# Kernel optimization log

Measured on AMD Instinct MI355X. Metric: run time of the kernel, lower is better.

The kernel has to match this reference:

```python
import jax, jax.numpy as jnp
import numpy as np

N_NODES = 50000
N_EDGES = 600000
D = 128


def setup_inputs() -> dict:
    key = jax.random.key(0)
    ks = jax.random.split(key, 8)
    s = 0.05
    return {
        "x": jax.random.normal(ks[0], (N_NODES, D), jnp.float32),
        "edge_index": jax.random.randint(ks[1], (2, N_EDGES), 0, N_NODES, jnp.int64),
        "edge_attr": jax.random.normal(ks[2], (N_EDGES, D), jnp.float32),
        "We1": jax.random.normal(ks[3], (3 * D, D), jnp.float32) * s,
        "be1": jnp.zeros((D,), jnp.float32),
        "We2": jax.random.normal(ks[4], (D, D), jnp.float32) * s,
        "be2": jnp.zeros((D,), jnp.float32),
        "Wn1": jax.random.normal(ks[5], (2 * D, D), jnp.float32) * s,
        "bn1": jnp.zeros((D,), jnp.float32),
        "Wn2": jax.random.normal(ks[6], (D, D), jnp.float32) * s,
        "bn2": jnp.zeros((D,), jnp.float32),
    }


def reference(x, edge_index, edge_attr, We1, be1, We2, be2, Wn1, bn1, Wn2, bn2):
    src = edge_index[0]
    dest = edge_index[1]
    n = x.shape[0]
    # edge model: MLP on [x_src | x_dest | edge_attr]  -> [E, D]
    e_in = jnp.concatenate([x[src], x[dest], edge_attr], axis=-1)
    e = jax.nn.relu(e_in @ We1 + be1) @ We2 + be2
    # node model: scatter-mean of updated edge_attr into dest nodes
    agg = jax.ops.segment_sum(e, dest, num_segments=n)
    cnt = jax.ops.segment_sum(jnp.ones((e.shape[0],), e.dtype), dest, num_segments=n)
    agg = agg / jnp.maximum(cnt, 1.0)[:, None]
    n_in = jnp.concatenate([x, agg], axis=-1)
    x_out = jax.nn.relu(n_in @ Wn1 + bn1) @ Wn2 + bn2
    return x_out, e
```

## Files before the change

kernel.cpp:

```cpp
#include <hip/hip_runtime.h>
#include <hip/hip_bf16.h>

#define DD 128

typedef short bf16x8 __attribute__((ext_vector_type(8)));
typedef float f32x4 __attribute__((ext_vector_type(4)));

__device__ __forceinline__ unsigned short f2b(float f) {
  unsigned int u = __float_as_uint(f);
  u = u + 0x7FFFu + ((u >> 16) & 1u);
  return (unsigned short)(u >> 16);
}
__device__ __forceinline__ float b2f(unsigned short u) {
  return __uint_as_float((unsigned int)u << 16);
}

__global__ void count_kernel(const int* __restrict__ ei, int* __restrict__ cnt, int E) {
  int i = blockIdx.x * blockDim.x + threadIdx.x;
  if (i < E) atomicAdd(&cnt[ei[E + i]], 1);
}

__global__ __launch_bounds__(256) void scan_a(const int* __restrict__ cnt,
                                              int* __restrict__ off,
                                              int* __restrict__ bsum, int N) {
  __shared__ int wsum[4];
  const int t = threadIdx.x;
  const int i0 = blockIdx.x * 1024 + t * 4;
  int4 v = {0, 0, 0, 0};
  if (i0 + 3 < N) v = *reinterpret_cast<const int4*>(cnt + i0);
  else {
    if (i0 < N)     v.x = cnt[i0];
    if (i0 + 1 < N) v.y = cnt[i0 + 1];
    if (i0 + 2 < N) v.z = cnt[i0 + 2];
    if (i0 + 3 < N) v.w = cnt[i0 + 3];
  }
  const int s1 = v.x, s2 = s1 + v.y, s3 = s2 + v.z, tot = s3 + v.w;
  const int lane = t & 63, wv = t >> 6;
  int sc = tot;
#pragma unroll
  for (int d = 1; d < 64; d <<= 1) {
    int u = __shfl_up(sc, d);
    if (lane >= d) sc += u;
  }
  if (lane == 63) wsum[wv] = sc;
  __syncthreads();
  int wpre = 0;
  for (int w = 0; w < wv; ++w) wpre += wsum[w];
  const int excl = wpre + sc - tot;
  if (i0 < N)     off[i0]     = excl;
  if (i0 + 1 < N) off[i0 + 1] = excl + s1;
  if (i0 + 2 < N) off[i0 + 2] = excl + s2;
  if (i0 + 3 < N) off[i0 + 3] = excl + s3;
  if (t == 255) bsum[blockIdx.x] = wpre + sc;
}

__global__ void scan_b(int* __restrict__ bsum, int B) {
  const int t = threadIdx.x;
  const int v0 = (t < B) ? bsum[t] : 0;
  int v = v0;
#pragma unroll
  for (int d = 1; d < 64; d <<= 1) {
    int u = __shfl_up(v, d);
    if (t >= d) v += u;
  }
  if (t < B) bsum[t] = v - v0;
}

__global__ __launch_bounds__(256) void scan_c(int* __restrict__ off, int* __restrict__ cur,
                                              const int* __restrict__ bsum, int N, int E) {
  const int t = threadIdx.x;
  const int add = bsum[blockIdx.x];
  const int i0 = blockIdx.x * 1024 + t * 4;
#pragma unroll
  for (int k = 0; k < 4; ++k) {
    const int i = i0 + k;
    if (i < N) {
      const int o = off[i] + add;
      off[i] = o;
      cur[i] = o;
    }
  }
  if (blockIdx.x == 0 && t == 0) off[N] = E;
}

__global__ void fill_kernel(const int* __restrict__ ei, int* __restrict__ cur,
                            int* __restrict__ perm, int E) {
  int i = blockIdx.x * blockDim.x + threadIdx.x;
  if (i < E) {
    const int d = ei[E + i];
    const int pos = atomicAdd(&cur[d], 1);
    perm[pos] = i;
  }
}

__global__ __launch_bounds__(256, 2) void pq_kernel(
    const float* __restrict__ x,
    const float* __restrict__ We1,
    unsigned short* __restrict__ pq,
    int N)
{
  __shared__ __align__(16) unsigned short x_lds[64][128];

  const int tid  = threadIdx.x;
  const int wv   = tid >> 6;
  const int lane = tid & 63;
  const int lg   = lane >> 4;
  const int lm   = lane & 15;

  bf16x8 wf[4][4];
#pragma unroll
  for (int nf = 0; nf < 4; ++nf) {
    const int n    = wv * 64 + nf * 16 + lm;
    const int col  = n & 127;
    const int kro  = (n >> 7) * 128;
#pragma unroll
    for (int kb = 0; kb < 4; ++kb) {
      bf16x8 f;
#pragma unroll
      for (int j = 0; j < 8; ++j)
        f[j] = (short)f2b(We1[(kro + kb * 32 + lg * 8 + j) * DD + col]);
      wf[kb][nf] = f;
    }
  }

  const int nbase = blockIdx.x * 64;

#pragma unroll
  for (int it = 0; it < 4; ++it) {
    const int q = tid + it * 256;
    const int r = q >> 4;
    const int c = q & 15;
    int gr = nbase + r; if (gr >= N) gr = N - 1;
    const float* p = x + (size_t)gr * DD + c * 8;
    const float4 va = *reinterpret_cast<const float4*>(p);
    const float4 vb = *reinterpret_cast<const float4*>(p + 4);
    bf16x8 o;
    o[0] = (short)f2b(va.x); o[1] = (short)f2b(va.y);
    o[2] = (short)f2b(va.z); o[3] = (short)f2b(va.w);
    o[4] = (short)f2b(vb.x); o[5] = (short)f2b(vb.y);
    o[6] = (short)f2b(vb.z); o[7] = (short)f2b(vb.w);
    *reinterpret_cast<bf16x8*>(&x_lds[r][(c ^ (r & 7)) * 8]) = o;
  }
  __syncthreads();

  f32x4 acc[4][4];
#pragma unroll
  for (int mf = 0; mf < 4; ++mf)
#pragma unroll
    for (int nf = 0; nf < 4; ++nf)
      acc[mf][nf] = (f32x4){0.f, 0.f, 0.f, 0.f};

#pragma unroll
  for (int kb = 0; kb < 4; ++kb) {
    bf16x8 a[4];
#pragma unroll
    for (int mf = 0; mf < 4; ++mf) {
      const int r = mf * 16 + lm;
      a[mf] = *reinterpret_cast<const bf16x8*>(&x_lds[r][((kb * 4 + lg) ^ (r & 7)) * 8]);
    }
#pragma unroll
    for (int mf = 0; mf < 4; ++mf)
#pragma unroll
      for (int nf = 0; nf < 4; ++nf)
        acc[mf][nf] = __builtin_amdgcn_mfma_f32_16x16x32_bf16(a[mf], wf[kb][nf], acc[mf][nf], 0, 0, 0);
  }

#pragma unroll
  for (int mf = 0; mf < 4; ++mf)
#pragma unroll
    for (int rg = 0; rg < 4; ++rg) {
      const int gm = nbase + mf * 16 + lg * 4 + rg;
      if (gm < N) {
#pragma unroll
        for (int nf = 0; nf < 4; ++nf)
          pq[(size_t)gm * 256 + wv * 64 + nf * 16 + lm] = f2b(acc[mf][nf][rg]);
      }
    }
}

__global__ __launch_bounds__(256, 3) void edge_mlp_kernel(
    const unsigned short* __restrict__ pq,
    const int* __restrict__ ei,
    const float* __restrict__ ea,
    const float* __restrict__ We1,
    const float* __restrict__ be1,
    const float* __restrict__ We2,
    const float* __restrict__ be2,
    float* __restrict__ e_out,
    int E)
{
  __shared__ __align__(16) unsigned short ea_lds[64][128];
  __shared__ __align__(16) unsigned short h_lds[64][136];
  __shared__ int srcs[64], dsts[64];

  const int tid  = threadIdx.x;
  const int wv   = tid >> 6;
  const int lane = tid & 63;
  const int lg   = lane >> 4;
  const int lm   = lane & 15;

  bf16x8 w1f[4][2];
  bf16x8 w2f[4][2];
  float b1[2], b2[2];
#pragma unroll
  for (int nf = 0; nf < 2; ++nf) {
    const int n = wv * 32 + nf * 16 + lm;
    b1[nf] = be1[n];
    b2[nf] = be2[n];
#pragma unroll
    for (int kb = 0; kb < 4; ++kb) {
      bf16x8 f;
#pragma unroll
      for (int j = 0; j < 8; ++j)
        f[j] = (short)f2b(We1[(256 + kb * 32 + lg * 8 + j) * DD + n]);
      w1f[kb][nf] = f;
    }
#pragma unroll
    for (int kb = 0; kb < 4; ++kb) {
      bf16x8 f;
#pragma unroll
      for (int j = 0; j < 8; ++j)
        f[j] = (short)f2b(We2[(kb * 32 + lg * 8 + j) * DD + n]);
      w2f[kb][nf] = f;
    }
  }

  const int ntiles = E >> 6;
  for (int tile = blockIdx.x; tile < ntiles; tile += gridDim.x) {
    const int ebase = tile << 6;
    __syncthreads();

    if (tid < 64)       srcs[tid]      = ei[ebase + tid];
    else if (tid < 128) dsts[tid - 64] = ei[E + ebase + tid - 64];
    __syncthreads();

    float4 va[4], vb[4];
#pragma unroll
    for (int it = 0; it < 4; ++it) {
      const int q = tid + it * 256;
      const float* p = ea + (size_t)(ebase + (q >> 4)) * DD + (q & 15) * 8;
      va[it] = *reinterpret_cast<const float4*>(p);
      vb[it] = *reinterpret_cast<const float4*>(p + 4);
    }

    f32x4 acc[4][2];
#pragma unroll
    for (int mf = 0; mf < 4; ++mf)
#pragma unroll
      for (int rg = 0; rg < 4; ++rg) {
        const int m = mf * 16 + lg * 4 + rg;
        const size_t rs = (size_t)srcs[m] * 256;
        const size_t rd = (size_t)dsts[m] * 256;
#pragma unroll
        for (int nf = 0; nf < 2; ++nf) {
          const int n = wv * 32 + nf * 16 + lm;
          acc[mf][nf][rg] = b2f(pq[rs + n]) + b2f(pq[rd + 128 + n]);
        }
      }

#pragma unroll
    for (int it = 0; it < 4; ++it) {
      const int q = tid + it * 256;
      const int r = q >> 4;
      const int c = q & 15;
      bf16x8 o;
      o[0] = (short)f2b(va[it].x); o[1] = (short)f2b(va[it].y);
      o[2] = (short)f2b(va[it].z); o[3] = (short)f2b(va[it].w);
      o[4] = (short)f2b(vb[it].x); o[5] = (short)f2b(vb[it].y);
      o[6] = (short)f2b(vb[it].z); o[7] = (short)f2b(vb[it].w);
      *reinterpret_cast<bf16x8*>(&ea_lds[r][(c ^ (r & 7)) * 8]) = o;
    }
    __syncthreads();

#pragma unroll
    for (int kb = 0; kb < 4; ++kb) {
      bf16x8 a[4];
#pragma unroll
      for (int mf = 0; mf < 4; ++mf) {
        const int r = mf * 16 + lm;
        a[mf] = *reinterpret_cast<const bf16x8*>(&ea_lds[r][((kb * 4 + lg) ^ (r & 7)) * 8]);
      }
#pragma unroll
      for (int mf = 0; mf < 4; ++mf)
#pragma unroll
        for (int nf = 0; nf < 2; ++nf)
          acc[mf][nf] = __builtin_amdgcn_mfma_f32_16x16x32_bf16(a[mf], w1f[kb][nf], acc[mf][nf], 0, 0, 0);
    }

#pragma unroll
    for (int mf = 0; mf < 4; ++mf)
#pragma unroll
      for (int nf = 0; nf < 2; ++nf)
#pragma unroll
        for (int rg = 0; rg < 4; ++rg) {
          const int m = mf * 16 + lg * 4 + rg;
          const int n = wv * 32 + nf * 16 + lm;
          float v = acc[mf][nf][rg] + b1[nf];
          h_lds[m][n] = f2b(v > 0.f ? v : 0.f);
        }
    __syncthreads();

    f32x4 acc2[4][2];
#pragma unroll
    for (int mf = 0; mf < 4; ++mf)
#pragma unroll
      for (int nf = 0; nf < 2; ++nf)
        acc2[mf][nf] = (f32x4){0.f, 0.f, 0.f, 0.f};

#pragma unroll
    for (int kb = 0; kb < 4; ++kb) {
      bf16x8 a[4];
#pragma unroll
      for (int mf = 0; mf < 4; ++mf)
        a[mf] = *reinterpret_cast<const bf16x8*>(&h_lds[mf * 16 + lm][kb * 32 + lg * 8]);
#pragma unroll
      for (int mf = 0; mf < 4; ++mf)
#pragma unroll
        for (int nf = 0; nf < 2; ++nf)
          acc2[mf][nf] = __builtin_amdgcn_mfma_f32_16x16x32_bf16(a[mf], w2f[kb][nf], acc2[mf][nf], 0, 0, 0);
    }

#pragma unroll
    for (int mf = 0; mf < 4; ++mf)
#pragma unroll
      for (int rg = 0; rg < 4; ++rg) {
        const int gm = ebase + mf * 16 + lg * 4 + rg;
#pragma unroll
        for (int nf = 0; nf < 2; ++nf) {
          const int n = wv * 32 + nf * 16 + lm;
          e_out[(size_t)gm * DD + n] = acc2[mf][nf][rg] + b2[nf];
        }
      }
  }
}

__global__ __launch_bounds__(256) void agg_kernel(const float* __restrict__ e_out,
                                                  const int* __restrict__ off,
                                                  const int* __restrict__ perm,
                                                  float* __restrict__ agg, int N) {
  const int wv   = threadIdx.x >> 6;
  const int lane = threadIdx.x & 63;
  const int nid  = blockIdx.x * 4 + wv;
  if (nid >= N) return;
  const int o0 = off[nid], o1 = off[nid + 1];
  float2 s0 = {0.f, 0.f}, s1 = {0.f, 0.f}, s2 = {0.f, 0.f}, s3 = {0.f, 0.f};
  int j = o0;
  for (; j + 4 <= o1; j += 4) {
    const int r0 = perm[j], r1 = perm[j + 1], r2 = perm[j + 2], r3 = perm[j + 3];
    const float2 v0 = *reinterpret_cast<const float2*>(e_out + (size_t)r0 * DD + (lane << 1));
    const float2 v1 = *reinterpret_cast<const float2*>(e_out + (size_t)r1 * DD + (lane << 1));
    const float2 v2 = *reinterpret_cast<const float2*>(e_out + (size_t)r2 * DD + (lane << 1));
    const float2 v3 = *reinterpret_cast<const float2*>(e_out + (size_t)r3 * DD + (lane << 1));
    s0.x += v0.x; s0.y += v0.y;
    s1.x += v1.x; s1.y += v1.y;
    s2.x += v2.x; s2.y += v2.y;
    s3.x += v3.x; s3.y += v3.y;
  }
  for (; j < o1; ++j) {
    const int r = perm[j];
    const float2 v = *reinterpret_cast<const float2*>(e_out + (size_t)r * DD + (lane << 1));
    s0.x += v.x; s0.y += v.y;
  }
  const int deg = o1 - o0;
  const float inv = deg > 0 ? 1.f / (float)deg : 0.f;
  float2 o;
  o.x = (s0.x + s1.x + s2.x + s3.x) * inv;
  o.y = (s0.y + s1.y + s2.y + s3.y) * inv;
  *reinterpret_cast<float2*>(agg + (size_t)nid * DD + (lane << 1)) = o;
}

__global__ __launch_bounds__(256, 2) void node_mlp_kernel(
    const float* __restrict__ x,
    const float* __restrict__ Wn1,
    const float* __restrict__ bn1,
    const float* __restrict__ Wn2,
    const float* __restrict__ bn2,
    float* __restrict__ xout,
    int N)
{
  __shared__ __align__(16) unsigned short A_lds[64][264];
  __shared__ __align__(16) unsigned short h_lds[64][136];

  const int tid  = threadIdx.x;
  const int wv   = tid >> 6;
  const int lane = tid & 63;
  const int lg   = lane >> 4;
  const int lm   = lane & 15;

  bf16x8 w1f[8][2];
  bf16x8 w2f[4][2];
  float b1[2], b2[2];
#pragma unroll
  for (int nf = 0; nf < 2; ++nf) {
    const int n = wv * 32 + nf * 16 + lm;
    b1[nf] = bn1[n];
    b2[nf] = bn2[n];
#pragma unroll
    for (int kb = 0; kb < 8; ++kb) {
      bf16x8 f;
#pragma unroll
      for (int j = 0; j < 8; ++j)
        f[j] = (short)f2b(Wn1[(kb * 32 + lg * 8 + j) * DD + n]);
      w1f[kb][nf] = f;
    }
#pragma unroll
    for (int kb = 0; kb < 4; ++kb) {
      bf16x8 f;
#pragma unroll
      for (int j = 0; j < 8; ++j)
        f[j] = (short)f2b(Wn2[(kb * 32 + lg * 8 + j) * DD + n]);
      w2f[kb][nf] = f;
    }
  }

  const int ntiles = (N + 63) >> 6;
  for (int tile = blockIdx.x; tile < ntiles; tile += gridDim.x) {
    const int nbase = tile << 6;
    __syncthreads();

#pragma unroll
    for (int it = 0; it < 16; ++it) {
      const int q = tid + it * 256;
      const int r = q >> 6;
      const int c = q & 63;
      int gr = nbase + r;
      if (gr >= N) gr = N - 1;
      float4 v;
      if (c < 32) v = *reinterpret_cast<const float4*>(x + (size_t)gr * DD + (c << 2));
      else        v = *reinterpret_cast<const float4*>(xout + (size_t)gr * DD + ((c - 32) << 2));
      unsigned short* dst = &A_lds[r][c << 2];
      dst[0] = f2b(v.x); dst[1] = f2b(v.y); dst[2] = f2b(v.z); dst[3] = f2b(v.w);
    }
    __syncthreads();

    f32x4 acc[4][2];
#pragma unroll
    for (int mf = 0; mf < 4; ++mf)
#pragma unroll
      for (int nf = 0; nf < 2; ++nf)
        acc[mf][nf] = (f32x4){0.f, 0.f, 0.f, 0.f};

#pragma unroll
    for (int kb = 0; kb < 8; ++kb) {
      bf16x8 a[4];
#pragma unroll
      for (int mf = 0; mf < 4; ++mf)
        a[mf] = *reinterpret_cast<const bf16x8*>(&A_lds[mf * 16 + lm][kb * 32 + lg * 8]);
#pragma unroll
      for (int mf = 0; mf < 4; ++mf)
#pragma unroll
        for (int nf = 0; nf < 2; ++nf)
          acc[mf][nf] = __builtin_amdgcn_mfma_f32_16x16x32_bf16(a[mf], w1f[kb][nf], acc[mf][nf], 0, 0, 0);
    }

#pragma unroll
    for (int mf = 0; mf < 4; ++mf)
#pragma unroll
      for (int nf = 0; nf < 2; ++nf)
#pragma unroll
        for (int rg = 0; rg < 4; ++rg) {
          const int m = mf * 16 + lg * 4 + rg;
          const int n = wv * 32 + nf * 16 + lm;
          float v = acc[mf][nf][rg] + b1[nf];
          h_lds[m][n] = f2b(v > 0.f ? v : 0.f);
        }
    __syncthreads();

    f32x4 acc2[4][2];
#pragma unroll
    for (int mf = 0; mf < 4; ++mf)
#pragma unroll
      for (int nf = 0; nf < 2; ++nf)
        acc2[mf][nf] = (f32x4){0.f, 0.f, 0.f, 0.f};

#pragma unroll
    for (int kb = 0; kb < 4; ++kb) {
      bf16x8 a[4];
#pragma unroll
      for (int mf = 0; mf < 4; ++mf)
        a[mf] = *reinterpret_cast<const bf16x8*>(&h_lds[mf * 16 + lm][kb * 32 + lg * 8]);
#pragma unroll
      for (int mf = 0; mf < 4; ++mf)
#pragma unroll
        for (int nf = 0; nf < 2; ++nf)
          acc2[mf][nf] = __builtin_amdgcn_mfma_f32_16x16x32_bf16(a[mf], w2f[kb][nf], acc2[mf][nf], 0, 0, 0);
    }

#pragma unroll
    for (int mf = 0; mf < 4; ++mf)
#pragma unroll
      for (int rg = 0; rg < 4; ++rg) {
        const int gm = nbase + mf * 16 + lg * 4 + rg;
        if (gm < N) {
#pragma unroll
          for (int nf = 0; nf < 2; ++nf) {
            const int n = wv * 32 + nf * 16 + lm;
            xout[(size_t)gm * DD + n] = acc2[mf][nf][rg] + b2[nf];
          }
        }
      }
  }
}

extern "C" void kernel_launch(void* const* d_in, const int* in_sizes, int n_in,
                              void* d_out, int out_size, void* d_ws, size_t ws_size,
                              hipStream_t stream) {
  const float* x   = (const float*)d_in[0];
  const int*   ei  = (const int*)d_in[1];
  const float* ea  = (const float*)d_in[2];
  const float* We1 = (const float*)d_in[3];
  const float* be1 = (const float*)d_in[4];
  const float* We2 = (const float*)d_in[5];
  const float* be2 = (const float*)d_in[6];
  const float* Wn1 = (const float*)d_in[7];
  const float* bn1 = (const float*)d_in[8];
  const float* Wn2 = (const float*)d_in[9];
  const float* bn2 = (const float*)d_in[10];

  const int N = in_sizes[0] / DD;
  const int E = in_sizes[2] / DD;

  float* out   = (float*)d_out;
  float* xout  = out;
  float* e_out = out + (size_t)N * DD;

  unsigned short* pq = (unsigned short*)xout;

  int* cnt  = (int*)d_ws;
  int* off  = cnt + N;
  int* cur  = off + N + 1;
  int* perm = cur + N;
  int* bsum = perm + E;

  const int SCAN_B = (N + 1023) / 1024;

  hipMemsetAsync(cnt, 0, (size_t)N * sizeof(int), stream);

  pq_kernel<<<(N + 63) / 64, 256, 0, stream>>>(x, We1, pq, N);

  count_kernel<<<(E + 255) / 256, 256, 0, stream>>>(ei, cnt, E);
  scan_a<<<SCAN_B, 256, 0, stream>>>(cnt, off, bsum, N);
  scan_b<<<1, 64, 0, stream>>>(bsum, SCAN_B);
  scan_c<<<SCAN_B, 256, 0, stream>>>(off, cur, bsum, N, E);
  fill_kernel<<<(E + 255) / 256, 256, 0, stream>>>(ei, cur, perm, E);

  edge_mlp_kernel<<<2048, 256, 0, stream>>>(pq, ei, ea, We1, be1, We2, be2, e_out, E);

  agg_kernel<<<(N + 3) / 4, 256, 0, stream>>>(e_out, off, perm, xout, N);

  const int node_tiles = (N + 63) / 64;
  node_mlp_kernel<<<node_tiles, 256, 0, stream>>>(x, Wn1, bn1, Wn2, bn2, xout, N);
}
```

Measured before the change: 401.5 us.

## Transpose edge MLP MFMA operands for vectorized gathers and stores, prefetch indices

Swaps the A and B operands of the edge-MLP MFMAs so each lane holds four consecutive output columns of one edge row. This lets the pq gathers, bias loads and e_out stores use 4-wide vector accesses instead of scalar ones. The hidden-activation LDS buffer now uses an XOR swizzle instead of padding. Edge indices are double-buffered and prefetched for the next tile, which drops one barrier per iteration. Edge-attribute loads move inline to cut register use, and occupancy is raised from 3 to 4 blocks per SM, which risks register spills.

```diff
diff --git a/kernel.cpp b/kernel.cpp
--- a/kernel.cpp
+++ b/kernel.cpp
@@ -4,6 +4,7 @@
 #define DD 128
 
 typedef short bf16x8 __attribute__((ext_vector_type(8)));
+typedef short bf16x4 __attribute__((ext_vector_type(4)));
 typedef float f32x4 __attribute__((ext_vector_type(4)));
 
 __device__ __forceinline__ unsigned short f2b(float f) {
@@ -178,7 +179,7 @@
     }
 }
 
-__global__ __launch_bounds__(256, 3) void edge_mlp_kernel(
+__global__ __launch_bounds__(256, 4) void edge_mlp_kernel(
     const unsigned short* __restrict__ pq,
     const int* __restrict__ ei,
     const float* __restrict__ ea,
@@ -190,8 +191,8 @@
     int E)
 {
   __shared__ __align__(16) unsigned short ea_lds[64][128];
-  __shared__ __align__(16) unsigned short h_lds[64][136];
-  __shared__ int srcs[64], dsts[64];
+  __shared__ __align__(16) unsigned short h_lds[64][128];
+  __shared__ int srcs[2][64], dsts[2][64];
 
   const int tid  = threadIdx.x;
   const int wv   = tid >> 6;
@@ -201,12 +202,12 @@
 
   bf16x8 w1f[4][2];
   bf16x8 w2f[4][2];
-  float b1[2], b2[2];
+  float4 b1v[2], b2v[2];
 #pragma unroll
   for (int nf = 0; nf < 2; ++nf) {
     const int n = wv * 32 + nf * 16 + lm;
-    b1[nf] = be1[n];
-    b2[nf] = be2[n];
+    b1v[nf] = *reinterpret_cast<const float4*>(&be1[wv * 32 + nf * 16 + 4 * lg]);
+    b2v[nf] = *reinterpret_cast<const float4*>(&be2[wv * 32 + nf * 16 + 4 * lg]);
 #pragma unroll
     for (int kb = 0; kb < 4; ++kb) {
       bf16x8 f;
@@ -226,49 +227,61 @@
   }
 
   const int ntiles = E >> 6;
-  for (int tile = blockIdx.x; tile < ntiles; tile += gridDim.x) {
+
+  {
+    const int t0 = blockIdx.x;
+    if (t0 < ntiles) {
+      const int eb = t0 << 6;
+      if (tid < 64)       srcs[0][tid]      = ei[eb + tid];
+      else if (tid < 128) dsts[0][tid - 64] = ei[E + eb + tid - 64];
+    }
+  }
+  __syncthreads();
+
+  int pb = 0;
+  for (int tile = blockIdx.x; tile < ntiles; tile += gridDim.x, pb ^= 1) {
     const int ebase = tile << 6;
-    __syncthreads();
-
-    if (tid < 64)       srcs[tid]      = ei[ebase + tid];
-    else if (tid < 128) dsts[tid - 64] = ei[E + ebase + tid - 64];
-    __syncthreads();
-
-    float4 va[4], vb[4];
-#pragma unroll
-    for (int it = 0; it < 4; ++it) {
-      const int q = tid + it * 256;
-      const float* p = ea + (size_t)(ebase + (q >> 4)) * DD + (q & 15) * 8;
-      va[it] = *reinterpret_cast<const float4*>(p);
-      vb[it] = *reinterpret_cast<const float4*>(p + 4);
-    }
 
     f32x4 acc[4][2];
 #pragma unroll
-    for (int mf = 0; mf < 4; ++mf)
-#pragma unroll
-      for (int rg = 0; rg < 4; ++rg) {
-        const int m = mf * 16 + lg * 4 + rg;
-        const size_t rs = (size_t)srcs[m] * 256;
-        const size_t rd = (size_t)dsts[m] * 256;
-#pragma unroll
-        for (int nf = 0; nf < 2; ++nf) {
-          const int n = wv * 32 + nf * 16 + lm;
-          acc[mf][nf][rg] = b2f(pq[rs + n]) + b2f(pq[rd + 128 + n]);
-        }
-      }
+    for (int mf = 0; mf < 4; ++mf) {
+      const size_t rs = (size_t)srcs[pb][mf * 16 + lm] * 256;
+      const size_t rd = (size_t)dsts[pb][mf * 16 + lm] * 256 + 128;
+#pragma unroll
+      for (int nf = 0; nf < 2; ++nf) {
+        const int n0 = wv * 32 + nf * 16 + 4 * lg;
+        const ushort4 pv = *reinterpret_cast<const ushort4*>(pq + rs + n0);
+        const ushort4 qv = *reinterpret_cast<const ushort4*>(pq + rd + n0);
+        acc[mf][nf][0] = b2f(pv.x) + b2f(qv.x);
+        acc[mf][nf][1] = b2f(pv.y) + b2f(qv.y);
+        acc[mf][nf][2] = b2f(pv.z) + b2f(qv.z);
+        acc[mf][nf][3] = b2f(pv.w) + b2f(qv.w);
+      }
+    }
 
 #pragma unroll
     for (int it = 0; it < 4; ++it) {
       const int q = tid + it * 256;
       const int r = q >> 4;
       const int c = q & 15;
+      const float* p = ea + (size_t)(ebase + r) * DD + c * 8;
+      const float4 va = *reinterpret_cast<const float4*>(p);
+      const float4 vb = *reinterpret_cast<const float4*>(p + 4);
       bf16x8 o;
-      o[0] = (short)f2b(va[it].x); o[1] = (short)f2b(va[it].y);
-      o[2] = (short)f2b(va[it].z); o[3] = (short)f2b(va[it].w);
-      o[4] = (short)f2b(vb[it].x); o[5] = (short)f2b(vb[it].y);
-      o[6] = (short)f2b(vb[it].z); o[7] = (short)f2b(vb[it].w);
+      o[0] = (short)f2b(va.x); o[1] = (short)f2b(va.y);
+      o[2] = (short)f2b(va.z); o[3] = (short)f2b(va.w);
+      o[4] = (short)f2b(vb.x); o[5] = (short)f2b(vb.y);
+      o[6] = (short)f2b(vb.z); o[7] = (short)f2b(vb.w);
       *reinterpret_cast<bf16x8*>(&ea_lds[r][(c ^ (r & 7)) * 8]) = o;
+    }
+
+    {
+      const int ntile = tile + gridDim.x;
+      if (ntile < ntiles) {
+        const int nb = ntile << 6;
+        if (tid < 64)       srcs[pb ^ 1][tid]      = ei[nb + tid];
+        else if (tid < 128) dsts[pb ^ 1][tid - 64] = ei[E + nb + tid - 64];
+      }
     }
     __syncthreads();
 
@@ -284,20 +297,26 @@
       for (int mf = 0; mf < 4; ++mf)
 #pragma unroll
         for (int nf = 0; nf < 2; ++nf)
-          acc[mf][nf] = __builtin_amdgcn_mfma_f32_16x16x32_bf16(a[mf], w1f[kb][nf], acc[mf][nf], 0, 0, 0);
-    }
-
-#pragma unroll
-    for (int mf = 0; mf < 4; ++mf)
-#pragma unroll
-      for (int nf = 0; nf < 2; ++nf)
+          acc[mf][nf] = __builtin_amdgcn_mfma_f32_16x16x32_bf16(w1f[kb][nf], a[mf], acc[mf][nf], 0, 0, 0);
+    }
+
+#pragma unroll
+    for (int mf = 0; mf < 4; ++mf) {
+      const int m = mf * 16 + lm;
+#pragma unroll
+      for (int nf = 0; nf < 2; ++nf) {
+        bf16x4 hv;
 #pragma unroll
         for (int rg = 0; rg < 4; ++rg) {
-          const int m = mf * 16 + lg * 4 + rg;
-          const int n = wv * 32 + nf * 16 + lm;
-          float v = acc[mf][nf][rg] + b1[nf];
-          h_lds[m][n] = f2b(v > 0.f ? v : 0.f);
+          const float bb = (rg == 0) ? b1v[nf].x : (rg == 1) ? b1v[nf].y
+                         : (rg == 2) ? b1v[nf].z : b1v[nf].w;
+          const float v = acc[mf][nf][rg] + bb;
+          hv[rg] = (short)f2b(v > 0.f ? v : 0.f);
         }
+        const int ch = (wv * 4 + nf * 2 + (lg >> 1)) ^ (m & 7);
+        *reinterpret_cast<bf16x4*>(&h_lds[m][ch * 8 + 4 * (lg & 1)]) = hv;
+      }
+    }
     __syncthreads();
 
     f32x4 acc2[4][2];
@@ -311,26 +330,31 @@
     for (int kb = 0; kb < 4; ++kb) {
       bf16x8 a[4];
 #pragma unroll
+      for (int mf = 0; mf < 4; ++mf) {
+        const int r = mf * 16 + lm;
+        a[mf] = *reinterpret_cast<const bf16x8*>(&h_lds[r][((kb * 4 + lg) ^ (r & 7)) * 8]);
+      }
+#pragma unroll
       for (int mf = 0; mf < 4; ++mf)
-        a[mf] = *reinterpret_cast<const bf16x8*>(&h_lds[mf * 16 + lm][kb * 32 + lg * 8]);
-#pragma unroll
-      for (int mf = 0; mf < 4; ++mf)
 #pragma unroll
         for (int nf = 0; nf < 2; ++nf)
-          acc2[mf][nf] = __builtin_amdgcn_mfma_f32_16x16x32_bf16(a[mf], w2f[kb][nf], acc2[mf][nf], 0, 0, 0);
-    }
-
-#pragma unroll
-    for (int mf = 0; mf < 4; ++mf)
-#pragma unroll
-      for (int rg = 0; rg < 4; ++rg) {
-        const int gm = ebase + mf * 16 + lg * 4 + rg;
-#pragma unroll
-        for (int nf = 0; nf < 2; ++nf) {
-          const int n = wv * 32 + nf * 16 + lm;
-          e_out[(size_t)gm * DD + n] = acc2[mf][nf][rg] + b2[nf];
-        }
-      }
+          acc2[mf][nf] = __builtin_amdgcn_mfma_f32_16x16x32_bf16(w2f[kb][nf], a[mf], acc2[mf][nf], 0, 0, 0);
+    }
+
+#pragma unroll
+    for (int mf = 0; mf < 4; ++mf) {
+      const int gm = ebase + mf * 16 + lm;
+#pragma unroll
+      for (int nf = 0; nf < 2; ++nf) {
+        float4 o;
+        o.x = acc2[mf][nf][0] + b2v[nf].x;
+        o.y = acc2[mf][nf][1] + b2v[nf].y;
+        o.z = acc2[mf][nf][2] + b2v[nf].z;
+        o.w = acc2[mf][nf][3] + b2v[nf].w;
+        *reinterpret_cast<float4*>(&e_out[(size_t)gm * DD + wv * 32 + nf * 16 + 4 * lg]) = o;
+      }
+    }
+    __syncthreads();
   }
 }
 
```

Result: slower. 501.5 us (+24.9%).

## Restructure edge MLP into per-wave 16-edge units with weights in LDS

Applied to the files above, without the earlier changes.

The edge MLP kernel now stores the transposed bf16 We1 (edge part) and We2 in swizzled LDS once per block. Each wave independently processes 16 edges, computing all 128 output columns, so the per-tile block-wide __syncthreads are gone. Edge attributes are loaded straight into registers as MFMA operands, and the first layer is computed transposed so the gathered pq rows load as vectors. This trades ~80KB of LDS per block (lower occupancy, launch bound 2, grid 512) for no block barriers and vectorized gathers.

```diff
diff --git a/kernel.cpp b/kernel.cpp
--- a/kernel.cpp
+++ b/kernel.cpp
@@ -4,6 +4,7 @@
 #define DD 128
 
 typedef short bf16x8 __attribute__((ext_vector_type(8)));
+typedef short bf16x4 __attribute__((ext_vector_type(4)));
 typedef float f32x4 __attribute__((ext_vector_type(4)));
 
 __device__ __forceinline__ unsigned short f2b(float f) {
@@ -178,7 +179,7 @@
     }
 }
 
-__global__ __launch_bounds__(256, 3) void edge_mlp_kernel(
+__global__ __launch_bounds__(256, 2) void edge_mlp_kernel(
     const unsigned short* __restrict__ pq,
     const int* __restrict__ ei,
     const float* __restrict__ ea,
@@ -189,148 +190,128 @@
     float* __restrict__ e_out,
     int E)
 {
-  __shared__ __align__(16) unsigned short ea_lds[64][128];
-  __shared__ __align__(16) unsigned short h_lds[64][136];
-  __shared__ int srcs[64], dsts[64];
+  __shared__ __align__(16) unsigned short w1T[128 * 128];
+  __shared__ __align__(16) unsigned short w2T[128 * 128];
+  __shared__ __align__(16) unsigned short h_lds[4][16 * 128];
 
   const int tid  = threadIdx.x;
   const int wv   = tid >> 6;
   const int lane = tid & 63;
   const int lg   = lane >> 4;
   const int lm   = lane & 15;
-
-  bf16x8 w1f[4][2];
-  bf16x8 w2f[4][2];
-  float b1[2], b2[2];
-#pragma unroll
-  for (int nf = 0; nf < 2; ++nf) {
-    const int n = wv * 32 + nf * 16 + lm;
-    b1[nf] = be1[n];
-    b2[nf] = be2[n];
+  const int swz  = lm & 7;
+
+  {
+    const int n  = tid & 127;
+    const int k0 = (tid >> 7) * 64;
+    for (int p = 0; p < 32; ++p) {
+      const int k = k0 + 2 * p;
+      const unsigned int w1p = (unsigned int)f2b(We1[(256 + k) * DD + n]) |
+                               ((unsigned int)f2b(We1[(257 + k) * DD + n]) << 16);
+      const unsigned int w2p = (unsigned int)f2b(We2[k * DD + n]) |
+                               ((unsigned int)f2b(We2[(k + 1) * DD + n]) << 16);
+      const int idx = n * 128 + (((k >> 3) ^ (n & 7)) << 3) + (k & 7);
+      *reinterpret_cast<unsigned int*>(&w1T[idx]) = w1p;
+      *reinterpret_cast<unsigned int*>(&w2T[idx]) = w2p;
+    }
+  }
+
+  float4 b1v[8];
+  float  b2s[8];
+#pragma unroll
+  for (int nf = 0; nf < 8; ++nf) {
+    b1v[nf] = *reinterpret_cast<const float4*>(&be1[nf * 16 + 4 * lg]);
+    b2s[nf] = be2[nf * 16 + lm];
+  }
+  __syncthreads();
+
+  unsigned short* hw = &h_lds[wv][0];
+
+  const int nunits  = E >> 4;
+  const int ustride = gridDim.x << 2;
+
+  for (int u = (blockIdx.x << 2) + wv; u < nunits; u += ustride) {
+    const int ebase = u << 4;
+    const int erow  = ebase + lm;
+    const int se = ei[erow];
+    const int de = ei[E + erow];
+
+    bf16x8 eaf[4];
+    const float* er = ea + (size_t)erow * DD;
 #pragma unroll
     for (int kb = 0; kb < 4; ++kb) {
-      bf16x8 f;
-#pragma unroll
-      for (int j = 0; j < 8; ++j)
-        f[j] = (short)f2b(We1[(256 + kb * 32 + lg * 8 + j) * DD + n]);
-      w1f[kb][nf] = f;
-    }
+      const float4 va = *reinterpret_cast<const float4*>(er + kb * 32 + lg * 8);
+      const float4 vb = *reinterpret_cast<const float4*>(er + kb * 32 + lg * 8 + 4);
+      bf16x8 o;
+      o[0] = (short)f2b(va.x); o[1] = (short)f2b(va.y);
+      o[2] = (short)f2b(va.z); o[3] = (short)f2b(va.w);
+      o[4] = (short)f2b(vb.x); o[5] = (short)f2b(vb.y);
+      o[6] = (short)f2b(vb.z); o[7] = (short)f2b(vb.w);
+      eaf[kb] = o;
+    }
+
+    f32x4 acc[8];
+    const unsigned short* pr = pq + (size_t)se * 256;
+    const unsigned short* qr = pq + (size_t)de * 256 + 128;
+#pragma unroll
+    for (int nf = 0; nf < 8; ++nf) {
+      const ushort4 pv = *reinterpret_cast<const ushort4*>(pr + nf * 16 + 4 * lg);
+      const ushort4 qv = *reinterpret_cast<const ushort4*>(qr + nf * 16 + 4 * lg);
+      acc[nf][0] = b2f(pv.x) + b2f(qv.x) + b1v[nf].x;
+      acc[nf][1] = b2f(pv.y) + b2f(qv.y) + b1v[nf].y;
+      acc[nf][2] = b2f(pv.z) + b2f(qv.z) + b1v[nf].z;
+      acc[nf][3] = b2f(pv.w) + b2f(qv.w) + b1v[nf].w;
+    }
+
 #pragma unroll
     for (int kb = 0; kb < 4; ++kb) {
-      bf16x8 f;
-#pragma unroll
-      for (int j = 0; j < 8; ++j)
-        f[j] = (short)f2b(We2[(kb * 32 + lg * 8 + j) * DD + n]);
-      w2f[kb][nf] = f;
-    }
-  }
-
-  const int ntiles = E >> 6;
-  for (int tile = blockIdx.x; tile < ntiles; tile += gridDim.x) {
-    const int ebase = tile << 6;
-    __syncthreads();
-
-    if (tid < 64)       srcs[tid]      = ei[ebase + tid];
-    else if (tid < 128) dsts[tid - 64] = ei[E + ebase + tid - 64];
-    __syncthreads();
-
-    float4 va[4], vb[4];
-#pragma unroll
-    for (int it = 0; it < 4; ++it) {
-      const int q = tid + it * 256;
-      const float* p = ea + (size_t)(ebase + (q >> 4)) * DD + (q & 15) * 8;
-      va[it] = *reinterpret_cast<const float4*>(p);
-      vb[it] = *reinterpret_cast<const float4*>(p + 4);
-    }
-
-    f32x4 acc[4][2];
-#pragma unroll
-    for (int mf = 0; mf < 4; ++mf)
+#pragma unroll
+      for (int nf = 0; nf < 8; ++nf) {
+        const bf16x8 wf = *reinterpret_cast<const bf16x8*>(
+            &w1T[(nf * 16 + lm) * 128 + (((kb * 4 + lg) ^ swz) << 3)]);
+        acc[nf] = __builtin_amdgcn_mfma_f32_16x16x32_bf16(wf, eaf[kb], acc[nf], 0, 0, 0);
+      }
+    }
+
+#pragma unroll
+    for (int nf = 0; nf < 8; ++nf) {
+      bf16x4 hv;
 #pragma unroll
       for (int rg = 0; rg < 4; ++rg) {
-        const int m = mf * 16 + lg * 4 + rg;
-        const size_t rs = (size_t)srcs[m] * 256;
-        const size_t rd = (size_t)dsts[m] * 256;
-#pragma unroll
-        for (int nf = 0; nf < 2; ++nf) {
-          const int n = wv * 32 + nf * 16 + lm;
-          acc[mf][nf][rg] = b2f(pq[rs + n]) + b2f(pq[rd + 128 + n]);
-        }
+        const float v = acc[nf][rg];
+        hv[rg] = (short)f2b(v > 0.f ? v : 0.f);
       }
-
-#pragma unroll
-    for (int it = 0; it < 4; ++it) {
-      const int q = tid + it * 256;
-      const int r = q >> 4;
-      const int c = q & 15;
-      bf16x8 o;
-      o[0] = (short)f2b(va[it].x); o[1] = (short)f2b(va[it].y);
-      o[2] = (short)f2b(va[it].z); o[3] = (short)f2b(va[it].w);
-      o[4] = (short)f2b(vb[it].x); o[5] = (short)f2b(vb[it].y);
-      o[6] = (short)f2b(vb[it].z); o[7] = (short)f2b(vb[it].w);
-      *reinterpret_cast<bf16x8*>(&ea_lds[r][(c ^ (r & 7)) * 8]) = o;
-    }
-    __syncthreads();
+      const int c8 = 2 * nf + (lg >> 1);
+      *reinterpret_cast<bf16x4*>(&hw[lm * 128 + ((c8 ^ swz) << 3) + 4 * (lg & 1)]) = hv;
+    }
+
+    bf16x8 hf[4];
+#pragma unroll
+    for (int kb = 0; kb < 4; ++kb)
+      hf[kb] = *reinterpret_cast<const bf16x8*>(
+          &hw[lm * 128 + (((kb * 4 + lg) ^ swz) << 3)]);
+
+    f32x4 acc2[8];
+#pragma unroll
+    for (int nf = 0; nf < 8; ++nf)
+      acc2[nf] = (f32x4){b2s[nf], b2s[nf], b2s[nf], b2s[nf]};
 
 #pragma unroll
     for (int kb = 0; kb < 4; ++kb) {
-      bf16x8 a[4];
-#pragma unroll
-      for (int mf = 0; mf < 4; ++mf) {
-        const int r = mf * 16 + lm;
-        a[mf] = *reinterpret_cast<const bf16x8*>(&ea_lds[r][((kb * 4 + lg) ^ (r & 7)) * 8]);
+#pragma unroll
+      for (int nf = 0; nf < 8; ++nf) {
+        const bf16x8 wf = *reinterpret_cast<const bf16x8*>(
+            &w2T[(nf * 16 + lm) * 128 + (((kb * 4 + lg) ^ swz) << 3)]);
+        acc2[nf] = __builtin_amdgcn_mfma_f32_16x16x32_bf16(hf[kb], wf, acc2[nf], 0, 0, 0);
       }
-#pragma unroll
-      for (int mf = 0; mf < 4; ++mf)
-#pragma unroll
-        for (int nf = 0; nf < 2; ++nf)
-          acc[mf][nf] = __builtin_amdgcn_mfma_f32_16x16x32_bf16(a[mf], w1f[kb][nf], acc[mf][nf], 0, 0, 0);
-    }
-
-#pragma unroll
-    for (int mf = 0; mf < 4; ++mf)
-#pragma unroll
-      for (int nf = 0; nf < 2; ++nf)
-#pragma unroll
-        for (int rg = 0; rg < 4; ++rg) {
-          const int m = mf * 16 + lg * 4 + rg;
-          const int n = wv * 32 + nf * 16 + lm;
-          float v = acc[mf][nf][rg] + b1[nf];
-          h_lds[m][n] = f2b(v > 0.f ? v : 0.f);
-        }
-    __syncthreads();
-
-    f32x4 acc2[4][2];
-#pragma unroll
-    for (int mf = 0; mf < 4; ++mf)
-#pragma unroll
-      for (int nf = 0; nf < 2; ++nf)
-        acc2[mf][nf] = (f32x4){0.f, 0.f, 0.f, 0.f};
-
-#pragma unroll
-    for (int kb = 0; kb < 4; ++kb) {
-      bf16x8 a[4];
-#pragma unroll
-      for (int mf = 0; mf < 4; ++mf)
-        a[mf] = *reinterpret_cast<const bf16x8*>(&h_lds[mf * 16 + lm][kb * 32 + lg * 8]);
-#pragma unroll
-      for (int mf = 0; mf < 4; ++mf)
-#pragma unroll
-        for (int nf = 0; nf < 2; ++nf)
-          acc2[mf][nf] = __builtin_amdgcn_mfma_f32_16x16x32_bf16(a[mf], w2f[kb][nf], acc2[mf][nf], 0, 0, 0);
-    }
-
-#pragma unroll
-    for (int mf = 0; mf < 4; ++mf)
-#pragma unroll
-      for (int rg = 0; rg < 4; ++rg) {
-        const int gm = ebase + mf * 16 + lg * 4 + rg;
-#pragma unroll
-        for (int nf = 0; nf < 2; ++nf) {
-          const int n = wv * 32 + nf * 16 + lm;
-          e_out[(size_t)gm * DD + n] = acc2[mf][nf][rg] + b2[nf];
-        }
-      }
+    }
+
+    float* eo = e_out + (size_t)(ebase + 4 * lg) * DD + lm;
+#pragma unroll
+    for (int rg = 0; rg < 4; ++rg)
+#pragma unroll
+      for (int nf = 0; nf < 8; ++nf)
+        eo[(size_t)rg * DD + nf * 16] = acc2[nf][rg];
   }
 }
 
@@ -544,7 +525,7 @@
   scan_c<<<SCAN_B, 256, 0, stream>>>(off, cur, bsum, N, E);
   fill_kernel<<<(E + 255) / 256, 256, 0, stream>>>(ei, cur, perm, E);
 
-  edge_mlp_kernel<<<2048, 256, 0, stream>>>(pq, ei, ea, We1, be1, We2, be2, e_out, E);
+  edge_mlp_kernel<<<512, 256, 0, stream>>>(pq, ei, ea, We1, be1, We2, be2, e_out, E);
 
   agg_kernel<<<(N + 3) / 4, 256, 0, stream>>>(e_out, off, perm, xout, N);
 
```

Result: slower. 652.5 us (+62.5%).

## Software-pipeline edge MLP tile loads and widen aggregation gather unroll

Applied to the files above, without the earlier changes.

The edge MLP loop now double-buffers the src/dest index arrays and prefetches the next tile's edge_attr into registers during the second GEMM, so global load latency overlaps with MFMA work. The pq gather is moved after the LDS barrier. Occupancy hint is raised from 3 to 4 blocks per CU, which may force register spills given the extra live prefetch registers. The aggregation kernel issues 8 independent gathers per iteration instead of 4, but sums into a single accumulator pair, which lengthens the dependent add chain.

```diff
diff --git a/kernel.cpp b/kernel.cpp
--- a/kernel.cpp
+++ b/kernel.cpp
@@ -178,7 +178,7 @@
     }
 }
 
-__global__ __launch_bounds__(256, 3) void edge_mlp_kernel(
+__global__ __launch_bounds__(256, 4) void edge_mlp_kernel(
     const unsigned short* __restrict__ pq,
     const int* __restrict__ ei,
     const float* __restrict__ ea,
@@ -191,7 +191,7 @@
 {
   __shared__ __align__(16) unsigned short ea_lds[64][128];
   __shared__ __align__(16) unsigned short h_lds[64][136];
-  __shared__ int srcs[64], dsts[64];
+  __shared__ int srcs[2][64], dsts[2][64];
 
   const int tid  = threadIdx.x;
   const int wv   = tid >> 6;
@@ -226,37 +226,34 @@
   }
 
   const int ntiles = E >> 6;
-  for (int tile = blockIdx.x; tile < ntiles; tile += gridDim.x) {
-    const int ebase = tile << 6;
-    __syncthreads();
-
-    if (tid < 64)       srcs[tid]      = ei[ebase + tid];
-    else if (tid < 128) dsts[tid - 64] = ei[E + ebase + tid - 64];
-    __syncthreads();
-
-    float4 va[4], vb[4];
+  const int stride = gridDim.x;
+
+  int tile = blockIdx.x;
+  float4 va[4], vb[4];
+  {
+    const int eb = tile << 6;
 #pragma unroll
     for (int it = 0; it < 4; ++it) {
       const int q = tid + it * 256;
-      const float* p = ea + (size_t)(ebase + (q >> 4)) * DD + (q & 15) * 8;
+      const float* p = ea + (size_t)(eb + (q >> 4)) * DD + (q & 15) * 8;
       va[it] = *reinterpret_cast<const float4*>(p);
       vb[it] = *reinterpret_cast<const float4*>(p + 4);
     }
-
-    f32x4 acc[4][2];
-#pragma unroll
-    for (int mf = 0; mf < 4; ++mf)
-#pragma unroll
-      for (int rg = 0; rg < 4; ++rg) {
-        const int m = mf * 16 + lg * 4 + rg;
-        const size_t rs = (size_t)srcs[m] * 256;
-        const size_t rd = (size_t)dsts[m] * 256;
-#pragma unroll
-        for (int nf = 0; nf < 2; ++nf) {
-          const int n = wv * 32 + nf * 16 + lm;
-          acc[mf][nf][rg] = b2f(pq[rs + n]) + b2f(pq[rd + 128 + n]);
-        }
-      }
+    if (tid < 64)       srcs[0][tid]      = ei[eb + tid];
+    else if (tid < 128) dsts[0][tid - 64] = ei[E + eb + tid - 64];
+  }
+  __syncthreads();
+
+  int pb = 0;
+  for (; tile < ntiles; tile += stride, pb ^= 1) {
+    const int ebase = tile << 6;
+    const int ntile = tile + stride;
+
+    if (ntile < ntiles) {
+      const int nb = ntile << 6;
+      if (tid < 64)       srcs[pb ^ 1][tid]      = ei[nb + tid];
+      else if (tid < 128) dsts[pb ^ 1][tid - 64] = ei[E + nb + tid - 64];
+    }
 
 #pragma unroll
     for (int it = 0; it < 4; ++it) {
@@ -272,6 +269,21 @@
     }
     __syncthreads();
 
+    f32x4 acc[4][2];
+#pragma unroll
+    for (int mf = 0; mf < 4; ++mf)
+#pragma unroll
+      for (int rg = 0; rg < 4; ++rg) {
+        const int m = mf * 16 + lg * 4 + rg;
+        const size_t rs = (size_t)srcs[pb][m] * 256;
+        const size_t rd = (size_t)dsts[pb][m] * 256;
+#pragma unroll
+        for (int nf = 0; nf < 2; ++nf) {
+          const int n = wv * 32 + nf * 16 + lm;
+          acc[mf][nf][rg] = b2f(pq[rs + n]) + b2f(pq[rd + 128 + n]);
+        }
+      }
+
 #pragma unroll
     for (int kb = 0; kb < 4; ++kb) {
       bf16x8 a[4];
@@ -299,6 +311,17 @@
           h_lds[m][n] = f2b(v > 0.f ? v : 0.f);
         }
     __syncthreads();
+
+    if (ntile < ntiles) {
+      const int nb = ntile << 6;
+#pragma unroll
+      for (int it = 0; it < 4; ++it) {
+        const int q = tid + it * 256;
+        const float* p = ea + (size_t)(nb + (q >> 4)) * DD + (q & 15) * 8;
+        va[it] = *reinterpret_cast<const float4*>(p);
+        vb[it] = *reinterpret_cast<const float4*>(p + 4);
+      }
+    }
 
     f32x4 acc2[4][2];
 #pragma unroll
@@ -343,29 +366,41 @@
   const int nid  = blockIdx.x * 4 + wv;
   if (nid >= N) return;
   const int o0 = off[nid], o1 = off[nid + 1];
-  float2 s0 = {0.f, 0.f}, s1 = {0.f, 0.f}, s2 = {0.f, 0.f}, s3 = {0.f, 0.f};
+  float sx = 0.f, sy = 0.f;
   int j = o0;
-  for (; j + 4 <= o1; j += 4) {
-    const int r0 = perm[j], r1 = perm[j + 1], r2 = perm[j + 2], r3 = perm[j + 3];
-    const float2 v0 = *reinterpret_cast<const float2*>(e_out + (size_t)r0 * DD + (lane << 1));
-    const float2 v1 = *reinterpret_cast<const float2*>(e_out + (size_t)r1 * DD + (lane << 1));
-    const float2 v2 = *reinterpret_cast<const float2*>(e_out + (size_t)r2 * DD + (lane << 1));
-    const float2 v3 = *reinterpret_cast<const float2*>(e_out + (size_t)r3 * DD + (lane << 1));
-    s0.x += v0.x; s0.y += v0.y;
-    s1.x += v1.x; s1.y += v1.y;
-    s2.x += v2.x; s2.y += v2.y;
-    s3.x += v3.x; s3.y += v3.y;
+  for (; j + 8 <= o1; j += 8) {
+    int r[8];
+#pragma unroll
+    for (int k = 0; k < 8; ++k) r[k] = perm[j + k];
+    float2 v[8];
+#pragma unroll
+    for (int k = 0; k < 8; ++k)
+      v[k] = *reinterpret_cast<const float2*>(e_out + (size_t)r[k] * DD + (lane << 1));
+#pragma unroll
+    for (int k = 0; k < 8; ++k) { sx += v[k].x; sy += v[k].y; }
+  }
+  if (j + 4 <= o1) {
+    int r[4];
+#pragma unroll
+    for (int k = 0; k < 4; ++k) r[k] = perm[j + k];
+    float2 v[4];
+#pragma unroll
+    for (int k = 0; k < 4; ++k)
+      v[k] = *reinterpret_cast<const float2*>(e_out + (size_t)r[k] * DD + (lane << 1));
+#pragma unroll
+    for (int k = 0; k < 4; ++k) { sx += v[k].x; sy += v[k].y; }
+    j += 4;
   }
   for (; j < o1; ++j) {
     const int r = perm[j];
     const float2 v = *reinterpret_cast<const float2*>(e_out + (size_t)r * DD + (lane << 1));
-    s0.x += v.x; s0.y += v.y;
+    sx += v.x; sy += v.y;
   }
   const int deg = o1 - o0;
   const float inv = deg > 0 ? 1.f / (float)deg : 0.f;
   float2 o;
-  o.x = (s0.x + s1.x + s2.x + s3.x) * inv;
-  o.y = (s0.y + s1.y + s2.y + s3.y) * inv;
+  o.x = sx * inv;
+  o.y = sy * inv;
   *reinterpret_cast<float2*>(agg + (size_t)nid * DD + (lane << 1)) = o;
 }
 
```

Result: slower. 510.5 us (+27.1%).
